# Kernel tuning notes

Hardware: AMD Instinct MI355X
Metric: run time of the kernel (lower is better)

## Reference

```python
import jax, jax.numpy as jnp
import numpy as np

B, S, D, NH, A, K, N_ITER = 512, 200, 512, 8, 512, 2, 3
DK = D // NH
L = 2 * K  # max local window length
NEG = -1e9


def make_pe_table(d, max_len):
    pos = np.arange(max_len)[:, None].astype(np.float64)
    j = np.arange(d)[None, :]
    ang = pos / np.power(10000.0, 2.0 * (j // 2) / d)
    pe = np.zeros((max_len, d))
    pe[:, 0::2] = np.sin(ang[:, 0::2])
    pe[:, 1::2] = np.cos(ang[:, 1::2])
    pe = np.concatenate([np.zeros((1, d)), pe], axis=0)  # pad row at index 0
    return jnp.asarray(pe, jnp.float32)


def layer_norm(x, g, b, eps=1e-5):
    m = jnp.mean(x, axis=-1, keepdims=True)
    v = jnp.mean((x - m) ** 2, axis=-1, keepdims=True)
    return (x - m) / jnp.sqrt(v + eps) * g + b


def setup_inputs() -> dict:
    key = jax.random.key(0)
    ks = jax.random.split(key, 24)
    p = lambda k, shape, s=0.02: jax.random.normal(k, shape, jnp.float32) * s
    embedded = jax.random.normal(ks[0], (B, S, D), jnp.float32)
    stc_lens = jax.random.randint(ks[1], (B,), 8, S + 1, jnp.int32)
    offsets = jnp.minimum(jax.random.randint(ks[2], (B,), 0, S, jnp.int32), stc_lens - 1)
    sep_lst = jnp.sort(jax.random.randint(ks[3], (B, 2), 0, S, jnp.int32), axis=1)
    return dict(
        embedded=embedded, stc_lens=stc_lens, offsets=offsets, sep_lst=sep_lst,
        W1=p(ks[4], (D, A)), W2=p(ks[5], (A, 1)),
        ln_g=jnp.ones((D,), jnp.float32), ln_b=jnp.zeros((D,), jnp.float32),
        lng_g=jnp.ones((D,), jnp.float32), lng_b=jnp.zeros((D,), jnp.float32),
        Wq=p(ks[6], (D, D)), bq=jnp.zeros((D,), jnp.float32),
        Wk=p(ks[7], (D, D)), bk=jnp.zeros((D,), jnp.float32),
        Wv=p(ks[8], (D, D)), bv=jnp.zeros((D,), jnp.float32),
        W_ih=p(ks[9], (3 * D, D)), W_hh=p(ks[10], (3 * D, D)),
        b_ih=jnp.zeros((3 * D,), jnp.float32), b_hh=jnp.zeros((3 * D,), jnp.float32),
        seg_emb=p(ks[11], (2, D)),
        pe_table=make_pe_table(D, S),
    )


def _forward(embedded, W1, W2, ln_g, ln_b, lng_g, lng_b, Wq, bq, Wk, bk, Wv, bv,
             W_ih, W_hh, b_ih, b_hh, seg_emb, pe_table, stc_lens, offsets, sep_lst):
    nsep = sep_lst.shape[1]
    bidx = jnp.arange(B)
    # ---- LocalVisiblePooling: per-sample window [start, end) around offset ----
    idx = jnp.sum(sep_lst < offsets[:, None], axis=1)  # segment index containing pos
    prev_sep = sep_lst[bidx, jnp.clip(idx - 1, 0, nsep - 1)]
    left = jnp.where(idx > 0, prev_sep + 1, 0)
    next_sep = sep_lst[bidx, jnp.clip(idx, 0, nsep - 1)]
    right = jnp.where(idx < nsep, next_sep, stc_lens)
    start = jnp.maximum(offsets - K, left)
    end = jnp.minimum(offsets + K, right)
    inds = start[:, None] + jnp.arange(L)  # [B, L]
    valid = inds < end[:, None]
    ic = jnp.clip(inds, 0, S - 1)
    h_blk = embedded[bidx[:, None], ic] * valid[..., None].astype(embedded.dtype)  # [B,L,D]
    a = jnp.tanh(h_blk @ W1) @ W2  # [B, L, 1]
    s1 = jax.nn.softmax(a[..., 0], axis=0)  # faithful to Softmax(dim=1) over batch dim
    score = jax.nn.softmax(jnp.where(valid, s1, NEG), axis=1)  # masked softmax over window
    b0_bf = jnp.einsum('bl,bld->bd', score, h_blk)  # [B, D]
    # ---- relative positional encoding for H ----
    x = jnp.arange(S)[None, :]  # [1, S]
    pos = offsets[:, None]
    ip = jnp.where(x < pos, pos - x, x + 1 - pos)
    ip = jnp.where(x < stc_lens[:, None], ip, 0)
    ip = jnp.clip(ip, 0, S)
    seg = (x >= pos).astype(jnp.int32)
    H = embedded + pe_table[ip] + seg_emb[seg]  # [B, S, D]
    H = layer_norm(H, ln_g, ln_b)
    b_t = layer_norm(b0_bf + pe_table[0], ln_g, ln_b)  # 'b' pe is the zero pad row
    # ---- GlobalUpdate: sigmoid-attention MHA (q_len=1) + GRUCell, N iterations ----
    pad = x >= stc_lens[:, None]  # [B, S] True where padded
    kproj = (H @ Wk + bk).reshape(B, S, NH, DK)
    vproj = (H @ Wv + bv).reshape(B, S, NH, DK)
    scale = 1.0 / jnp.sqrt(jnp.float32(DK))
    for _ in range(N_ITER):
        q = (b_t @ Wq + bq).reshape(B, NH, DK)
        scores = jnp.einsum('bhd,bshd->bhs', q, kproj) * scale
        scores = jnp.where(pad[:, None, :], NEG, scores)
        p_attn = jax.nn.sigmoid(scores)  # non-standard sigmoid attention
        m_t = jnp.einsum('bhs,bshd->bhd', p_attn, vproj).reshape(B, D)
        m_t = layer_norm(m_t, lng_g, lng_b)
        gi = m_t @ W_ih.T + b_ih
        gh = b_t @ W_hh.T + b_hh
        ir, iz, inn = jnp.split(gi, 3, axis=-1)
        hr, hz, hn = jnp.split(gh, 3, axis=-1)
        r = jax.nn.sigmoid(ir + hr)
        z = jax.nn.sigmoid(iz + hz)
        n = jnp.tanh(inn + r * hn)
        b_t = (1.0 - z) * n + z * b_t
    return b_t[:, None, :]  # [B, 1, D]


def reference(embedded, stc_lens, offsets, sep_lst, W1, W2, ln_g, ln_b, lng_g, lng_b,
              Wq, bq, Wk, bk, Wv, bv, W_ih, W_hh, b_ih, b_hh, seg_emb, pe_table):
    return _forward(embedded, W1, W2, ln_g, ln_b, lng_g, lng_b, Wq, bq, Wk, bk, Wv, bv,
                    W_ih, W_hh, b_ih, b_hh, seg_emb, pe_table, stc_lens, offsets, sep_lst)
```

## Files before the change

### kernel.cpp

```cpp
#include <hip/hip_runtime.h>
#include <hip/hip_bf16.h>
#include <math.h>

constexpr int B_   = 512;
constexpr int S_   = 200;
constexpr int D_   = 512;
constexpr int LBLK = 4;
constexpr int NITER = 3;
constexpr int TD_  = 1536;
#define NEGV (-1000000000.0f)

using bf16 = __hip_bfloat16;
typedef __attribute__((ext_vector_type(8))) short bf16x8;
typedef __attribute__((ext_vector_type(4))) float f32x4;

__device__ __forceinline__ float wred(float x) {
#pragma unroll
    for (int o = 32; o; o >>= 1) x += __shfl_xor(x, o);
    return x;
}

__device__ __forceinline__ void gload16(const bf16* g, bf16* l) {
    __builtin_amdgcn_global_load_lds(
        (const __attribute__((address_space(1))) void*)g,
        (__attribute__((address_space(3))) void*)l, 16, 0, 0);
}

__global__ void __launch_bounds__(256) k_prep(
        const float* __restrict__ Wq, const float* __restrict__ Wk,
        const float* __restrict__ Wv, const float* __restrict__ bk,
        const float* __restrict__ bv, const float* __restrict__ Wih,
        const float* __restrict__ Whh, bf16* __restrict__ WqT,
        bf16* __restrict__ WkvT, float* __restrict__ bkv,
        bf16* __restrict__ Wih_b, bf16* __restrict__ Whh_b) {
    int i = blockIdx.x * 256 + threadIdx.x;
    if (i < 512 * 512) {
        int n = i >> 9, k = i & 511;
        WqT[i] = __float2bfloat16(Wq[k * 512 + n]);
        return;
    }
    i -= 512 * 512;
    if (i < 1024 * 512) {
        int n = i >> 9, k = i & 511;
        WkvT[i] = __float2bfloat16(n < 512 ? Wk[k * 512 + n]
                                           : Wv[k * 512 + (n - 512)]);
        return;
    }
    i -= 1024 * 512;
    if (i < TD_ * D_) { Wih_b[i] = __float2bfloat16(Wih[i]); return; }
    i -= TD_ * D_;
    if (i < TD_ * D_) { Whh_b[i] = __float2bfloat16(Whh[i]); return; }
    i -= TD_ * D_;
    if (i < 1024) bkv[i] = (i < 512) ? bk[i] : bv[i - 512];
}

__global__ void __launch_bounds__(256) k_blockscore(
        const float* __restrict__ emb, const float* __restrict__ W1,
        const float* __restrict__ W2, const int* __restrict__ stc,
        const int* __restrict__ offs, const int* __restrict__ sep,
        float* __restrict__ hblk, float* __restrict__ a_out,
        int* __restrict__ se_out) {
    int b = blockIdx.x;
    int t = threadIdx.x;
    int off = offs[b], slen = stc[b];
    int sA = sep[b * 2 + 0], sB = sep[b * 2 + 1];
    int idx = (sA < off ? 1 : 0) + (sB < off ? 1 : 0);
    int prev = (idx == 2) ? sB : sA;
    int nxt  = (idx == 0) ? sA : sB;
    int left = (idx > 0) ? prev + 1 : 0;
    int right = (idx < 2) ? nxt : slen;
    int start = max(off - 2, left);
    int end   = min(off + 2, right);

    __shared__ float hs[LBLK][D_];
    {
        int l = t >> 6, lane = t & 63;
        int ind = start + l;
        bool valid = ind < end;
        float v0x=0,v0y=0,v0z=0,v0w=0,v1x=0,v1y=0,v1z=0,v1w=0;
        if (valid) {
            int ic = min(max(ind, 0), S_ - 1);
            const float* src = emb + ((size_t)b * S_ + ic) * D_ + lane * 8;
            float4 u0 = *(const float4*)src;
            float4 u1 = *(const float4*)(src + 4);
            v0x=u0.x; v0y=u0.y; v0z=u0.z; v0w=u0.w;
            v1x=u1.x; v1y=u1.y; v1z=u1.z; v1w=u1.w;
        }
        int base = lane * 8;
        hs[l][base+0]=v0x; hs[l][base+1]=v0y; hs[l][base+2]=v0z; hs[l][base+3]=v0w;
        hs[l][base+4]=v1x; hs[l][base+5]=v1y; hs[l][base+6]=v1z; hs[l][base+7]=v1w;
        float* g = hblk + ((size_t)b * LBLK + l) * D_ + base;
        g[0]=v0x; g[1]=v0y; g[2]=v0z; g[3]=v0w; g[4]=v1x; g[5]=v1y; g[6]=v1z; g[7]=v1w;
    }
    __syncthreads();

    float pa0 = 0.f, pa1 = 0.f, pa2 = 0.f, pa3 = 0.f;
#pragma unroll
    for (int cc = 0; cc < 2; ++cc) {
        int col = t + cc * 256;
        float a0 = 0.f, a1 = 0.f, a2 = 0.f, a3 = 0.f;
        for (int d = 0; d < D_; ++d) {
            float w = W1[(size_t)d * 512 + col];
            a0 += hs[0][d] * w; a1 += hs[1][d] * w;
            a2 += hs[2][d] * w; a3 += hs[3][d] * w;
        }
        float w2 = W2[col];
        pa0 += tanhf(a0) * w2; pa1 += tanhf(a1) * w2;
        pa2 += tanhf(a2) * w2; pa3 += tanhf(a3) * w2;
    }
    __shared__ float red[256];
    float pv[4] = {pa0, pa1, pa2, pa3};
#pragma unroll
    for (int l = 0; l < 4; ++l) {
        red[t] = pv[l]; __syncthreads();
        for (int st = 128; st; st >>= 1) {
            if (t < st) red[t] += red[t + st];
            __syncthreads();
        }
        if (t == 0) a_out[b * 4 + l] = red[0];
        __syncthreads();
    }
    if (t == 0) { se_out[b * 2] = start; se_out[b * 2 + 1] = end; }
}

__global__ void __launch_bounds__(512) k_score(const float* __restrict__ a_in,
                                               const int* __restrict__ se,
                                               float* __restrict__ score) {
    int b = threadIdx.x;
    float av[4], s1[4];
#pragma unroll
    for (int l = 0; l < 4; ++l) av[l] = a_in[b * 4 + l];
    __shared__ float red[512];
#pragma unroll
    for (int l = 0; l < 4; ++l) {
        red[b] = av[l]; __syncthreads();
        for (int st = 256; st; st >>= 1) {
            if (b < st) red[b] = fmaxf(red[b], red[b + st]);
            __syncthreads();
        }
        float mx = red[0]; __syncthreads();
        float e = expf(av[l] - mx);
        red[b] = e; __syncthreads();
        for (int st = 256; st; st >>= 1) {
            if (b < st) red[b] += red[b + st];
            __syncthreads();
        }
        s1[l] = e / red[0];
        __syncthreads();
    }
    int start = se[b * 2], end = se[b * 2 + 1];
    float x[4], mx2 = -1e30f;
#pragma unroll
    for (int l = 0; l < 4; ++l) {
        x[l] = (start + l < end) ? s1[l] : NEGV;
        mx2 = fmaxf(mx2, x[l]);
    }
    float s = 0.f, e4[4];
#pragma unroll
    for (int l = 0; l < 4; ++l) { e4[l] = expf(x[l] - mx2); s += e4[l]; }
    float inv = 1.f / s;
#pragma unroll
    for (int l = 0; l < 4; ++l) score[b * 4 + l] = e4[l] * inv;
}

__global__ void __launch_bounds__(64) k_b0(
        const float* __restrict__ hblk, const float* __restrict__ score,
        const float* __restrict__ pe, const float* __restrict__ g,
        const float* __restrict__ bb, float* __restrict__ bt,
        bf16* __restrict__ btb) {
    int b = blockIdx.x, lane = threadIdx.x;
    float sc0 = score[b*4+0], sc1 = score[b*4+1], sc2 = score[b*4+2], sc3 = score[b*4+3];
    const float* hb = hblk + (size_t)b * LBLK * D_ + lane * 8;
    float v[8];
#pragma unroll
    for (int j = 0; j < 8; ++j) {
        float x = pe[lane * 8 + j];
        x += sc0 * hb[j] + sc1 * hb[D_ + j] + sc2 * hb[2*D_ + j] + sc3 * hb[3*D_ + j];
        v[j] = x;
    }
    float sum = 0.f;
#pragma unroll
    for (int j = 0; j < 8; ++j) sum += v[j];
    sum = wred(sum);
    float mean = sum * (1.f / 512.f);
    float sq = 0.f;
#pragma unroll
    for (int j = 0; j < 8; ++j) { float c = v[j] - mean; sq += c * c; }
    sq = wred(sq);
    float rstd = rsqrtf(sq * (1.f / 512.f) + 1e-5f);
#pragma unroll
    for (int j = 0; j < 8; ++j) {
        int d = lane * 8 + j;
        float y = (v[j] - mean) * rstd * g[d] + bb[d];
        bt[(size_t)b * D_ + d] = y;
        btb[(size_t)b * D_ + d] = __float2bfloat16(y);
    }
}

__global__ void __launch_bounds__(256) k_H(
        const float* __restrict__ emb, const float* __restrict__ pe,
        const float* __restrict__ seg_emb, const float* __restrict__ g,
        const float* __restrict__ bb, const int* __restrict__ stc,
        const int* __restrict__ offs, bf16* __restrict__ Hc,
        int b0, int nrows) {
    int rid = blockIdx.x * 4 + (threadIdx.x >> 6);
    if (rid >= nrows) return;
    int lane = threadIdx.x & 63;
    int bl = rid / S_;
    int s = rid - bl * S_;
    int b = b0 + bl;
    int slen = stc[b];
    if (s >= slen) return;
    int pos = offs[b];
    int ip = (s < pos) ? (pos - s) : (s + 1 - pos);
    if (ip > S_) ip = S_;
    int seg = (s >= pos) ? 1 : 0;
    const float* er = emb + ((size_t)b * S_ + s) * D_ + lane * 8;
    const float* pr = pe + (size_t)ip * D_ + lane * 8;
    const float* sr = seg_emb + seg * D_ + lane * 8;
    float4 e0 = *(const float4*)er, e1 = *(const float4*)(er + 4);
    float4 p0 = *(const float4*)pr, p1 = *(const float4*)(pr + 4);
    float4 q0 = *(const float4*)sr, q1 = *(const float4*)(sr + 4);
    float v[8];
    v[0]=e0.x+p0.x+q0.x; v[1]=e0.y+p0.y+q0.y; v[2]=e0.z+p0.z+q0.z; v[3]=e0.w+p0.w+q0.w;
    v[4]=e1.x+p1.x+q1.x; v[5]=e1.y+p1.y+q1.y; v[6]=e1.z+p1.z+q1.z; v[7]=e1.w+p1.w+q1.w;
    float sum = 0.f;
#pragma unroll
    for (int j = 0; j < 8; ++j) sum += v[j];
    sum = wred(sum);
    float mean = sum * (1.f / 512.f);
    float sq = 0.f;
#pragma unroll
    for (int j = 0; j < 8; ++j) { float c = v[j] - mean; sq += c * c; }
    sq = wred(sq);
    float rstd = rsqrtf(sq * (1.f / 512.f) + 1e-5f);
    union { uint4 u; bf16 h[8]; } o;
#pragma unroll
    for (int j = 0; j < 8; ++j) {
        int d = lane * 8 + j;
        o.h[j] = __float2bfloat16((v[j] - mean) * rstd * g[d] + bb[d]);
    }
    *(uint4*)(Hc + ((size_t)bl * S_ + s) * D_ + lane * 8) = o.u;
}

template<int BM, int BN, int NWM, int NWN, bool OUT_BF16>
__device__ __forceinline__ void gemm_core(
        const bf16* __restrict__ A, int lda,
        const bf16* __restrict__ Bnk, int ldb,
        const float* __restrict__ bias,
        void* __restrict__ Cout, int ldc, int rows_valid) {
    constexpr int NW = NWM * NWN;
    constexpr int FM = BM / (NWM * 16);
    constexpr int FN = BN / (NWN * 16);
    constexpr int IA = BM / (16 * NW);
    constexpr int IB = BN / (16 * NW);
    __shared__ bf16 As[BM * 32];
    __shared__ bf16 Bs[BN * 32];
    int t = threadIdx.x, lane = t & 63, w = t >> 6;
    int wm = w / NWN, wn = w % NWN;
    int sr = lane >> 2;
    int sc = (lane & 3) * 8;

    f32x4 acc[FM][FN];
#pragma unroll
    for (int i = 0; i < FM; ++i)
#pragma unroll
        for (int j = 0; j < FN; ++j) acc[i][j] = f32x4{0.f,0.f,0.f,0.f};

    for (int k0 = 0; k0 < 512; k0 += 32) {
#pragma unroll
        for (int j = 0; j < IA; ++j) {
            int r = (w * IA + j) * 16 + sr;
            gload16(A + (size_t)r * lda + k0 + sc, &As[(w * IA + j) * 512]);
        }
#pragma unroll
        for (int j = 0; j < IB; ++j) {
            int r = (w * IB + j) * 16 + sr;
            gload16(Bnk + (size_t)r * ldb + k0 + sc, &Bs[(w * IB + j) * 512]);
        }
        __syncthreads();
        bf16x8 af[FM], bfr[FN];
#pragma unroll
        for (int i = 0; i < FM; ++i)
            af[i] = *(const bf16x8*)&As[((wm * FM + i) * 16 + (lane & 15)) * 32
                                        + (lane >> 4) * 8];
#pragma unroll
        for (int j = 0; j < FN; ++j)
            bfr[j] = *(const bf16x8*)&Bs[((wn * FN + j) * 16 + (lane & 15)) * 32
                                         + (lane >> 4) * 8];
#pragma unroll
        for (int i = 0; i < FM; ++i)
#pragma unroll
            for (int j = 0; j < FN; ++j)
                acc[i][j] = __builtin_amdgcn_mfma_f32_16x16x32_bf16(
                                af[i], bfr[j], acc[i][j], 0, 0, 0);
        __syncthreads();
    }
    int coln = wn * FN * 16 + (lane & 15);
    int rowb = (lane >> 4) * 4;
#pragma unroll
    for (int j = 0; j < FN; ++j) {
        int col = coln + j * 16;
        float bvv = bias[col];
#pragma unroll
        for (int i = 0; i < FM; ++i) {
            int rbase = (wm * FM + i) * 16 + rowb;
#pragma unroll
            for (int rr = 0; rr < 4; ++rr) {
                int row = rbase + rr;
                if (row < rows_valid) {
                    float v = acc[i][j][rr] + bvv;
                    if (OUT_BF16)
                        ((bf16*)Cout)[(size_t)row * ldc + col] = __float2bfloat16(v);
                    else
                        ((float*)Cout)[(size_t)row * ldc + col] = v;
                }
            }
        }
    }
}

__global__ void __launch_bounds__(256) k_gemm_kv2(
        const bf16* __restrict__ Hc, const bf16* __restrict__ WkvT,
        const float* __restrict__ bkv, bf16* __restrict__ kv,
        const int* __restrict__ stc, int b0) {
    int bl = blockIdx.z;
    int b = b0 + bl;
    int s0 = blockIdx.y * 64;
    int slen = stc[b];
    if (s0 >= slen) return;
    int n0 = blockIdx.x * 256;
    gemm_core<64, 256, 1, 4, true>(
        Hc + ((size_t)bl * S_ + s0) * D_, D_,
        WkvT + (size_t)n0 * 512, 512, bkv + n0,
        kv + ((size_t)b * S_ + s0) * 1024 + n0, 1024,
        min(64, slen - s0));
}

__global__ void __launch_bounds__(256) k_gemm_q(
        const bf16* __restrict__ btb, const bf16* __restrict__ WqT,
        const float* __restrict__ bq, float* __restrict__ qb) {
    int n0 = blockIdx.x * 64, m0 = blockIdx.y * 64;
    gemm_core<64, 64, 2, 2, false>(
        btb + (size_t)m0 * D_, D_, WqT + (size_t)n0 * 512, 512, bq + n0,
        qb + (size_t)m0 * D_ + n0, D_, 64);
}

__global__ void __launch_bounds__(256) k_gemm_gates(
        const bf16* __restrict__ mb, const bf16* __restrict__ btb,
        const bf16* __restrict__ Wih_b, const bf16* __restrict__ Whh_b,
        const float* __restrict__ b_ih, const float* __restrict__ b_hh,
        float* __restrict__ gi, float* __restrict__ gh) {
    int n0 = blockIdx.x * 128, m0 = blockIdx.y * 64;
    const bf16* A  = blockIdx.z ? btb : mb;
    const bf16* Bm = blockIdx.z ? Whh_b : Wih_b;
    const float* bias = blockIdx.z ? b_hh : b_ih;
    float* C = blockIdx.z ? gh : gi;
    gemm_core<64, 128, 2, 2, false>(
        A + (size_t)m0 * D_, D_, Bm + (size_t)n0 * 512, 512, bias + n0,
        C + (size_t)m0 * TD_ + n0, TD_, 64);
}

__global__ void __launch_bounds__(256) k_attn(
        const float* __restrict__ q, const bf16* __restrict__ kv,
        const int* __restrict__ stc, const float* __restrict__ lng_g,
        const float* __restrict__ lng_b, float* __restrict__ mf,
        bf16* __restrict__ mb) {
    int b = blockIdx.x;
    int t = threadIdx.x, w = t >> 6, lane = t & 63;
    int slen = stc[b];
    const float* qp = q + (size_t)b * D_ + lane * 8;
    float4 qa = *(const float4*)qp, qb4 = *(const float4*)(qp + 4);
    float qv[8] = {qa.x, qa.y, qa.z, qa.w, qb4.x, qb4.y, qb4.z, qb4.w};
    float acc[8] = {0,0,0,0,0,0,0,0};
    const bf16* kvb = kv + (size_t)b * S_ * 1024 + lane * 8;
    for (int s = w; s < slen; s += 4) {
        union { uint4 u; bf16 h[8]; } kl, vl;
        kl.u = *(const uint4*)(kvb + (size_t)s * 1024);
        float part = 0.f;
#pragma unroll
        for (int j = 0; j < 8; ++j) part += qv[j] * __bfloat162float(kl.h[j]);
        part += __shfl_xor(part, 1);
        part += __shfl_xor(part, 2);
        part += __shfl_xor(part, 4);
        float p = 1.f / (1.f + __expf(-part * 0.125f));
        vl.u = *(const uint4*)(kvb + (size_t)s * 1024 + 512);
#pragma unroll
        for (int j = 0; j < 8; ++j) acc[j] += p * __bfloat162float(vl.h[j]);
    }
    __shared__ float macc[4][D_];
#pragma unroll
    for (int j = 0; j < 8; ++j) macc[w][lane * 8 + j] = acc[j];
    __syncthreads();
    __shared__ float red[256];
    int d1 = t + 256;
    float x0 = macc[0][t] + macc[1][t] + macc[2][t] + macc[3][t];
    float x1 = macc[0][d1] + macc[1][d1] + macc[2][d1] + macc[3][d1];
    red[t] = x0 + x1; __syncthreads();
    for (int st = 128; st; st >>= 1) {
        if (t < st) red[t] += red[t + st];
        __syncthreads();
    }
    float mean = red[0] * (1.f / 512.f); __syncthreads();
    float c0 = x0 - mean, c1 = x1 - mean;
    red[t] = c0 * c0 + c1 * c1; __syncthreads();
    for (int st = 128; st; st >>= 1) {
        if (t < st) red[t] += red[t + st];
        __syncthreads();
    }
    float rstd = rsqrtf(red[0] * (1.f / 512.f) + 1e-5f);
    float y0 = c0 * rstd * lng_g[t] + lng_b[t];
    float y1 = c1 * rstd * lng_g[d1] + lng_b[d1];
    mf[(size_t)b * D_ + t] = y0;
    mf[(size_t)b * D_ + d1] = y1;
    mb[(size_t)b * D_ + t] = __float2bfloat16(y0);
    mb[(size_t)b * D_ + d1] = __float2bfloat16(y1);
}

__global__ void __launch_bounds__(256) k_gru(
        const float* __restrict__ gi, const float* __restrict__ gh,
        float* __restrict__ bt, bf16* __restrict__ btb) {
    int i = blockIdx.x * 256 + threadIdx.x;
    int b = i >> 9, d = i & 511;
    const float* gib = gi + (size_t)b * TD_;
    const float* ghb = gh + (size_t)b * TD_;
    float ir = gib[d], iz = gib[512 + d], inn = gib[1024 + d];
    float hr = ghb[d], hz = ghb[512 + d], hn = ghb[1024 + d];
    float r = 1.f / (1.f + expf(-(ir + hr)));
    float z = 1.f / (1.f + expf(-(iz + hz)));
    float n = tanhf(inn + r * hn);
    float bo = bt[i];
    float bn = (1.f - z) * n + z * bo;
    bt[i] = bn;
    btb[i] = __float2bfloat16(bn);
}

extern "C" void kernel_launch(void* const* d_in, const int* in_sizes, int n_in,
                              void* d_out, int out_size, void* d_ws, size_t ws_size,
                              hipStream_t stream) {
    const float* emb   = (const float*)d_in[0];
    const int*   stc   = (const int*)d_in[1];
    const int*   offs  = (const int*)d_in[2];
    const int*   sep   = (const int*)d_in[3];
    const float* W1    = (const float*)d_in[4];
    const float* W2    = (const float*)d_in[5];
    const float* ln_g  = (const float*)d_in[6];
    const float* ln_b  = (const float*)d_in[7];
    const float* lng_g = (const float*)d_in[8];
    const float* lng_b = (const float*)d_in[9];
    const float* Wq    = (const float*)d_in[10];
    const float* bq    = (const float*)d_in[11];
    const float* Wk    = (const float*)d_in[12];
    const float* bk    = (const float*)d_in[13];
    const float* Wv    = (const float*)d_in[14];
    const float* bv    = (const float*)d_in[15];
    const float* W_ih  = (const float*)d_in[16];
    const float* W_hh  = (const float*)d_in[17];
    const float* b_ih  = (const float*)d_in[18];
    const float* b_hh  = (const float*)d_in[19];
    const float* seg_e = (const float*)d_in[20];
    const float* pe    = (const float*)d_in[21];

    char* base = (char*)d_ws;
    size_t off = 0;
    auto alloc = [&](size_t bytes) -> void* {
        off = (off + 255) & ~(size_t)255;
        void* r = base + off;
        off += bytes;
        return r;
    };
    bf16* kv   = (bf16*)alloc(((size_t)B_ * S_ + 64) * 1024 * 2);
    float* hblk = (float*)alloc((size_t)B_ * LBLK * D_ * 4);
    float* a_s  = (float*)alloc((size_t)B_ * 4 * 4);
    float* scr  = (float*)alloc((size_t)B_ * 4 * 4);
    int*   se   = (int*)alloc((size_t)B_ * 2 * 4);
    float* bt   = (float*)alloc((size_t)B_ * D_ * 4);
    bf16*  btb  = (bf16*)alloc((size_t)B_ * D_ * 2);
    float* qb   = (float*)alloc((size_t)B_ * D_ * 4);
    float* mf   = (float*)alloc((size_t)B_ * D_ * 4);
    bf16*  mb   = (bf16*)alloc((size_t)B_ * D_ * 2);
    float* gi   = (float*)alloc((size_t)B_ * TD_ * 4);
    float* gh   = (float*)alloc((size_t)B_ * TD_ * 4);
    bf16* WqT   = (bf16*)alloc((size_t)D_ * D_ * 2);
    bf16* WkvT  = (bf16*)alloc((size_t)1024 * 512 * 2);
    float* bkv  = (float*)alloc((size_t)1024 * 4);
    bf16* Wih_b = (bf16*)alloc((size_t)TD_ * D_ * 2);
    bf16* Whh_b = (bf16*)alloc((size_t)TD_ * D_ * 2);

    auto hbytes = [](int ch) { return ((size_t)ch * S_ + 64) * D_ * 2; };
    int CH = 512;
    {
        size_t used = (off + 255) & ~(size_t)255;
        size_t remain = (ws_size > used) ? (ws_size - used) : 0;
        if (hbytes(512) + 256 > remain) CH = 64;
        if (CH == 64 && hbytes(64) + 256 > remain) CH = 16;
    }
    bf16* Hc = (bf16*)alloc(hbytes(CH));

    {
        int total = 512*512 + 1024*512 + 2*TD_*D_ + 1024;
        k_prep<<<(total + 255) / 256, 256, 0, stream>>>(
            Wq, Wk, Wv, bk, bv, W_ih, W_hh, WqT, WkvT, bkv, Wih_b, Whh_b);
    }

    k_blockscore<<<B_, 256, 0, stream>>>(emb, W1, W2, stc, offs, sep, hblk, a_s, se);
    k_score<<<1, 512, 0, stream>>>(a_s, se, scr);
    k_b0<<<B_, 64, 0, stream>>>(hblk, scr, pe, ln_g, ln_b, bt, btb);

    for (int c = 0; c < B_; c += CH) {
        int rows = CH * S_;
        k_H<<<(rows + 3) / 4, 256, 0, stream>>>(emb, pe, seg_e, ln_g, ln_b,
                                                stc, offs, Hc, c, rows);
        k_gemm_kv2<<<dim3(4, 4, CH), 256, 0, stream>>>(Hc, WkvT, bkv, kv, stc, c);
    }

    for (int it = 0; it < NITER; ++it) {
        k_gemm_q<<<dim3(8, 8), 256, 0, stream>>>(btb, WqT, bq, qb);
        k_attn<<<B_, 256, 0, stream>>>(qb, kv, stc, lng_g, lng_b, mf, mb);
        k_gemm_gates<<<dim3(12, 8, 2), 256, 0, stream>>>(mb, btb, Wih_b, Whh_b,
                                                         b_ih, b_hh, gi, gh);
        k_gru<<<(B_ * D_) / 256, 256, 0, stream>>>(gi, gh, bt, btb);
    }
    hipMemcpyAsync(d_out, bt, (size_t)out_size * sizeof(float),
                   hipMemcpyDeviceToDevice, stream);
}
```

Before: 783.2 us.

## Rewrite GEMM core with double-buffered swizzled LDS, 128x128 tiles, staged epilogue

Replaces the shared GEMM routine with a version that double-buffers K=64 slices in LDS, so the next slice's global-to-LDS load overlaps the current slice's MFMA work. LDS rows use an XOR swizzle to cut bank conflicts. All three GEMMs move to 128x128 tiles. The epilogue now writes results through LDS and stores them as coalesced 16-byte chunks. The cost is larger LDS use per block and far fewer blocks for the small Q and gate GEMMs, which may leave many CUs idle.

```diff
diff --git a/kernel.cpp b/kernel.cpp
--- a/kernel.cpp
+++ b/kernel.cpp
@@ -243,23 +243,27 @@
     *(uint4*)(Hc + ((size_t)bl * S_ + s) * D_ + lane * 8) = o.u;
 }
 
-template<int BM, int BN, int NWM, int NWN, bool OUT_BF16>
-__device__ __forceinline__ void gemm_core(
+template<int BM, int BN, bool OUT_BF16>
+__device__ __forceinline__ void gemm_core2(
         const bf16* __restrict__ A, int lda,
         const bf16* __restrict__ Bnk, int ldb,
         const float* __restrict__ bias,
         void* __restrict__ Cout, int ldc, int rows_valid) {
-    constexpr int NW = NWM * NWN;
-    constexpr int FM = BM / (NWM * 16);
-    constexpr int FN = BN / (NWN * 16);
-    constexpr int IA = BM / (16 * NW);
-    constexpr int IB = BN / (16 * NW);
-    __shared__ bf16 As[BM * 32];
-    __shared__ bf16 Bs[BN * 32];
+    constexpr int NW = 4, NWN = 2;
+    constexpr int FM = BM / 32;
+    constexpr int FN = BN / 32;
+    constexpr int IA = BM / (8 * NW);
+    constexpr int IB = BN / (8 * NW);
+    constexpr int SMEM_B = 2 * (BM + BN) * 64 * 2;
+    __shared__ char smem[SMEM_B];
+    bf16* As = (bf16*)smem;
+    bf16* Bs = (bf16*)(smem + 2 * BM * 64 * 2);
+
     int t = threadIdx.x, lane = t & 63, w = t >> 6;
     int wm = w / NWN, wn = w % NWN;
-    int sr = lane >> 2;
-    int sc = (lane & 3) * 8;
+    int srow = lane >> 3;
+    int scol = ((lane & 7) ^ srow) * 8;
+    int fr = lane & 15, q0 = lane >> 4;
 
     f32x4 acc[FM][FN];
 #pragma unroll
@@ -267,56 +271,84 @@
 #pragma unroll
         for (int j = 0; j < FN; ++j) acc[i][j] = f32x4{0.f,0.f,0.f,0.f};
 
-    for (int k0 = 0; k0 < 512; k0 += 32) {
-#pragma unroll
-        for (int j = 0; j < IA; ++j) {
-            int r = (w * IA + j) * 16 + sr;
-            gload16(A + (size_t)r * lda + k0 + sc, &As[(w * IA + j) * 512]);
-        }
-#pragma unroll
-        for (int j = 0; j < IB; ++j) {
-            int r = (w * IB + j) * 16 + sr;
-            gload16(Bnk + (size_t)r * ldb + k0 + sc, &Bs[(w * IB + j) * 512]);
-        }
+    auto STAGE = [&](int buf, int k0) {
+#pragma unroll
+        for (int jj = 0; jj < IA; ++jj) {
+            int g = w * IA + jj;
+            gload16(A + (size_t)(g * 8 + srow) * lda + k0 + scol,
+                    As + buf * BM * 64 + g * 512);
+        }
+#pragma unroll
+        for (int jj = 0; jj < IB; ++jj) {
+            int g = w * IB + jj;
+            gload16(Bnk + (size_t)(g * 8 + srow) * ldb + k0 + scol,
+                    Bs + buf * BN * 64 + g * 512);
+        }
+    };
+    auto COMPUTE = [&](int buf) {
+#pragma unroll
+        for (int h = 0; h < 2; ++h) {
+            bf16x8 af[FM], bf_[FN];
+#pragma unroll
+            for (int i = 0; i < FM; ++i) {
+                int R = (wm * FM + i) * 16 + fr;
+                int slot = (h * 4 + q0) ^ (R & 7);
+                af[i] = *(const bf16x8*)&As[buf * BM * 64 + R * 64 + slot * 8];
+            }
+#pragma unroll
+            for (int j = 0; j < FN; ++j) {
+                int R = (wn * FN + j) * 16 + fr;
+                int slot = (h * 4 + q0) ^ (R & 7);
+                bf_[j] = *(const bf16x8*)&Bs[buf * BN * 64 + R * 64 + slot * 8];
+            }
+#pragma unroll
+            for (int i = 0; i < FM; ++i)
+#pragma unroll
+                for (int j = 0; j < FN; ++j)
+                    acc[i][j] = __builtin_amdgcn_mfma_f32_16x16x32_bf16(
+                                    af[i], bf_[j], acc[i][j], 0, 0, 0);
+        }
+    };
+
+    STAGE(0, 0);
+    __syncthreads();
+    int cur = 0;
+#pragma unroll
+    for (int kt = 1; kt < 8; ++kt) {
+        STAGE(cur ^ 1, kt * 64);
+        COMPUTE(cur);
         __syncthreads();
-        bf16x8 af[FM], bfr[FN];
-#pragma unroll
-        for (int i = 0; i < FM; ++i)
-            af[i] = *(const bf16x8*)&As[((wm * FM + i) * 16 + (lane & 15)) * 32
-                                        + (lane >> 4) * 8];
-#pragma unroll
-        for (int j = 0; j < FN; ++j)
-            bfr[j] = *(const bf16x8*)&Bs[((wn * FN + j) * 16 + (lane & 15)) * 32
-                                         + (lane >> 4) * 8];
-#pragma unroll
-        for (int i = 0; i < FM; ++i)
-#pragma unroll
-            for (int j = 0; j < FN; ++j)
-                acc[i][j] = __builtin_amdgcn_mfma_f32_16x16x32_bf16(
-                                af[i], bfr[j], acc[i][j], 0, 0, 0);
-        __syncthreads();
-    }
-    int coln = wn * FN * 16 + (lane & 15);
-    int rowb = (lane >> 4) * 4;
+        cur ^= 1;
+    }
+    COMPUTE(cur);
+    __syncthreads();
+
+    constexpr int ESZ = OUT_BF16 ? 2 : 4;
 #pragma unroll
     for (int j = 0; j < FN; ++j) {
-        int col = coln + j * 16;
-        float bvv = bias[col];
+        int Cc = (wn * FN + j) * 16 + fr;
+        float bvv = bias[Cc];
 #pragma unroll
         for (int i = 0; i < FM; ++i) {
-            int rbase = (wm * FM + i) * 16 + rowb;
+            int Rb = (wm * FM + i) * 16 + q0 * 4;
 #pragma unroll
             for (int rr = 0; rr < 4; ++rr) {
-                int row = rbase + rr;
-                if (row < rows_valid) {
-                    float v = acc[i][j][rr] + bvv;
-                    if (OUT_BF16)
-                        ((bf16*)Cout)[(size_t)row * ldc + col] = __float2bfloat16(v);
-                    else
-                        ((float*)Cout)[(size_t)row * ldc + col] = v;
-                }
+                float v = acc[i][j][rr] + bvv;
+                if (OUT_BF16)
+                    ((bf16*)smem)[(Rb + rr) * BN + Cc] = __float2bfloat16(v);
+                else
+                    ((float*)smem)[(size_t)(Rb + rr) * BN + Cc] = v;
             }
         }
+    }
+    __syncthreads();
+    constexpr int CPR = BN * ESZ / 16;
+#pragma unroll 2
+    for (int c = t; c < BM * CPR; c += NW * 64) {
+        int row = c / CPR, ch = c - row * CPR;
+        if (row < rows_valid)
+            *(uint4*)((char*)Cout + (size_t)row * ldc * ESZ + ch * 16) =
+                *(const uint4*)(smem + (size_t)c * 16);
     }
 }
 
@@ -326,24 +358,24 @@
         const int* __restrict__ stc, int b0) {
     int bl = blockIdx.z;
     int b = b0 + bl;
-    int s0 = blockIdx.y * 64;
+    int s0 = blockIdx.y * 128;
     int slen = stc[b];
     if (s0 >= slen) return;
-    int n0 = blockIdx.x * 256;
-    gemm_core<64, 256, 1, 4, true>(
+    int n0 = blockIdx.x * 128;
+    gemm_core2<128, 128, true>(
         Hc + ((size_t)bl * S_ + s0) * D_, D_,
         WkvT + (size_t)n0 * 512, 512, bkv + n0,
         kv + ((size_t)b * S_ + s0) * 1024 + n0, 1024,
-        min(64, slen - s0));
+        min(128, slen - s0));
 }
 
 __global__ void __launch_bounds__(256) k_gemm_q(
         const bf16* __restrict__ btb, const bf16* __restrict__ WqT,
         const float* __restrict__ bq, float* __restrict__ qb) {
-    int n0 = blockIdx.x * 64, m0 = blockIdx.y * 64;
-    gemm_core<64, 64, 2, 2, false>(
+    int n0 = blockIdx.x * 128, m0 = blockIdx.y * 128;
+    gemm_core2<128, 128, false>(
         btb + (size_t)m0 * D_, D_, WqT + (size_t)n0 * 512, 512, bq + n0,
-        qb + (size_t)m0 * D_ + n0, D_, 64);
+        qb + (size_t)m0 * D_ + n0, D_, 128);
 }
 
 __global__ void __launch_bounds__(256) k_gemm_gates(
@@ -351,14 +383,14 @@
         const bf16* __restrict__ Wih_b, const bf16* __restrict__ Whh_b,
         const float* __restrict__ b_ih, const float* __restrict__ b_hh,
         float* __restrict__ gi, float* __restrict__ gh) {
-    int n0 = blockIdx.x * 128, m0 = blockIdx.y * 64;
+    int n0 = blockIdx.x * 128, m0 = blockIdx.y * 128;
     const bf16* A  = blockIdx.z ? btb : mb;
     const bf16* Bm = blockIdx.z ? Whh_b : Wih_b;
     const float* bias = blockIdx.z ? b_hh : b_ih;
     float* C = blockIdx.z ? gh : gi;
-    gemm_core<64, 128, 2, 2, false>(
+    gemm_core2<128, 128, false>(
         A + (size_t)m0 * D_, D_, Bm + (size_t)n0 * 512, 512, bias + n0,
-        C + (size_t)m0 * TD_ + n0, TD_, 64);
+        C + (size_t)m0 * TD_ + n0, TD_, 128);
 }
 
 __global__ void __launch_bounds__(256) k_attn(
@@ -511,13 +543,13 @@
         int rows = CH * S_;
         k_H<<<(rows + 3) / 4, 256, 0, stream>>>(emb, pe, seg_e, ln_g, ln_b,
                                                 stc, offs, Hc, c, rows);
-        k_gemm_kv2<<<dim3(4, 4, CH), 256, 0, stream>>>(Hc, WkvT, bkv, kv, stc, c);
+        k_gemm_kv2<<<dim3(8, 2, CH), 256, 0, stream>>>(Hc, WkvT, bkv, kv, stc, c);
     }
 
     for (int it = 0; it < NITER; ++it) {
-        k_gemm_q<<<dim3(8, 8), 256, 0, stream>>>(btb, WqT, bq, qb);
+        k_gemm_q<<<dim3(4, 4), 256, 0, stream>>>(btb, WqT, bq, qb);
         k_attn<<<B_, 256, 0, stream>>>(qb, kv, stc, lng_g, lng_b, mf, mb);
-        k_gemm_gates<<<dim3(12, 8, 2), 256, 0, stream>>>(mb, btb, Wih_b, Whh_b,
+        k_gemm_gates<<<dim3(12, 4, 2), 256, 0, stream>>>(mb, btb, Wih_b, Whh_b,
                                                          b_ih, b_hh, gi, gh);
         k_gru<<<(B_ * D_) / 256, 256, 0, stream>>>(gi, gh, bt, btb);
     }
```

New measurement: 717.0 us. -8.5%, faster.
